# Kernel optimization log

Hardware: AMD Instinct MI355X
Metric: run time of the kernel (lower is better)

The kernel has to match this reference:

```python
import jax, jax.numpy as jnp
import numpy as np
import math

B = 2000000
TWO_PI = 2.0 * math.pi

# ---- e3nn so3 generator construction (numpy, done once at import) ----

def _su2_generators(j):
    m = np.arange(-j, j)
    raising = np.diag(-np.sqrt(j * (j + 1) - m * (m + 1)), k=-1).astype(np.complex128)
    m = np.arange(-j + 1, j + 1)
    lowering = np.diag(np.sqrt(j * (j + 1) - m * (m - 1)), k=1).astype(np.complex128)
    m = np.arange(-j, j + 1)
    return np.stack([0.5 * (raising + lowering), np.diag(1j * m), -0.5j * (raising - lowering)])

def _change_basis_real_to_complex(l):
    q = np.zeros((2 * l + 1, 2 * l + 1), dtype=np.complex128)
    for m in range(-l, 0):
        q[l + m, l + abs(m)] = 1 / 2 ** 0.5
        q[l + m, l - abs(m)] = -1j / 2 ** 0.5
    q[l, l] = 1
    for m in range(1, l + 1):
        q[l + m, l + abs(m)] = (-1) ** m / 2 ** 0.5
        q[l + m, l - abs(m)] = 1j * (-1) ** m / 2 ** 0.5
    return (-1j) ** l * q

def _so3_generators(l):
    X = _su2_generators(l)
    Q = _change_basis_real_to_complex(l)
    return np.real(np.conj(Q.T) @ X @ Q)  # (3, 2l+1, 2l+1); X[0]=x-gen, X[1]=y-gen

def _eig_decomp(X):
    # X real antisymmetric with exact eigenvalues i*m; exp(a*X) = V diag(e^{a w}) V^-1
    w, V = np.linalg.eig(X.astype(np.complex128))
    w = 1j * np.round(w.imag)  # snap to exact i*m
    Vinv = np.linalg.inv(V)
    return (jnp.asarray(w, jnp.complex64), jnp.asarray(V, jnp.complex64), jnp.asarray(Vinv, jnp.complex64))

_GEN = {}
for _l in (4, 6):
    _X = _so3_generators(_l)
    _GEN[_l] = (_eig_decomp(_X[1]), _eig_decomp(_X[0]))  # (y-generator, x-generator)

# ---- rotations / angles (e3nn conventions) ----

def _quat_to_matrix(q):
    # e3nn: angle = 2*acos(clamp(w)), axis = normalize(q[1:]), Rodrigues
    angle = 2.0 * jnp.arccos(jnp.clip(q[..., 0], -1.0, 1.0))
    axis = q[..., 1:]
    axis = axis / jnp.maximum(jnp.linalg.norm(axis, axis=-1, keepdims=True), 1e-12)
    x, y, z = axis[..., 0], axis[..., 1], axis[..., 2]
    c, s = jnp.cos(angle), jnp.sin(angle)
    C = 1.0 - c
    return jnp.stack([
        jnp.stack([c + x * x * C, x * y * C - z * s, x * z * C + y * s], -1),
        jnp.stack([y * x * C + z * s, c + y * y * C, y * z * C - x * s], -1),
        jnp.stack([z * x * C - y * s, z * y * C + x * s, c + z * z * C], -1),
    ], -2)

def _matrix_y(a):
    c, s = jnp.cos(a), jnp.sin(a)
    o, z = jnp.ones_like(a), jnp.zeros_like(a)
    return jnp.stack([jnp.stack([c, z, s], -1), jnp.stack([z, o, z], -1), jnp.stack([-s, z, c], -1)], -2)

def _matrix_x(a):
    c, s = jnp.cos(a), jnp.sin(a)
    o, z = jnp.ones_like(a), jnp.zeros_like(a)
    return jnp.stack([jnp.stack([o, z, z], -1), jnp.stack([z, c, -s], -1), jnp.stack([z, s, c], -1)], -2)

def _xyz_to_angles(xyz):
    n = jnp.linalg.norm(xyz, axis=-1, keepdims=True)
    xyz = jnp.clip(xyz / jnp.maximum(n, 1e-12), -1.0, 1.0)
    beta = jnp.arccos(xyz[..., 1])
    alpha = jnp.arctan2(xyz[..., 0], xyz[..., 2])
    return alpha, beta

def _matrix_to_angles(R):
    x = R[..., :, 1]  # R @ [0,1,0]
    a, b = _xyz_to_angles(x)
    M = jnp.swapaxes(_matrix_y(a) @ _matrix_x(b), -1, -2) @ R
    c = jnp.arctan2(M[..., 0, 2], M[..., 0, 0])
    return a, b, c

# ---- Wigner-D applied to a fixed vector (fused matvec chain) ----

def _rot_apply(decomp, angle, v):
    # exp(angle*X) @ v via precomputed eigendecomposition; result is real
    w, V, Vinv = decomp
    u = jnp.einsum('mj,bj->bm', Vinv, v.astype(jnp.complex64))
    u = u * jnp.exp(angle[:, None].astype(jnp.complex64) * w)
    return jnp.real(jnp.einsum('im,bm->bi', V, u))

def _wigner_apply(l, alpha, beta, gamma, s):
    # D_l(alpha,beta,gamma) @ s = exp(a*Y) exp(b*X) exp(g*Y) @ s
    dy, dx = _GEN[l]
    v = jnp.broadcast_to(s, (alpha.shape[0], s.shape[0]))
    v = _rot_apply(dy, gamma % TWO_PI, v)
    v = _rot_apply(dx, beta % TWO_PI, v)
    v = _rot_apply(dy, alpha % TWO_PI, v)
    return v


def setup_inputs() -> dict:
    key = jax.random.key(0)
    k1, k2, k3 = jax.random.split(key, 3)
    quats = jax.random.normal(k1, (B, 4), dtype=jnp.float32)
    quats = quats / jnp.linalg.norm(quats, axis=-1, keepdims=True)  # unit quaternions
    s4 = jax.random.normal(k2, (9,), dtype=jnp.float32)
    s6 = jax.random.normal(k3, (13,), dtype=jnp.float32)
    return {"quats": quats, "s4": s4, "s6": s6}


def reference(quats, s4, s6):
    R = _quat_to_matrix(quats)
    alpha, beta, gamma = _matrix_to_angles(R)
    f4 = _wigner_apply(4, alpha, beta, gamma, s4)  # (B, 9)
    f6 = _wigner_apply(6, alpha, beta, gamma, s6)  # (B, 13)
    return (f4, f6)
```

## Files before the change

### kernel.cpp

```cpp
#include <hip/hip_runtime.h>
#include <math.h>

#define INV_SQRT2 0.70710678118654752440
#define PI_D 3.14159265358979323846

__global__ void build_J(float* __restrict__ ws) {
  const int l = (blockIdx.x == 0) ? 4 : 6;
  const int n = 2 * l + 1;
  const int off = (blockIdx.x == 0) ? 0 : 96;
  const int tid = threadIdx.x;
  __shared__ double Qr[169], Qi[169], Br[169], Bi[169], A[169], T[169], U[169];

  for (int t = tid; t < 169; t += blockDim.x) { Qr[t] = 0.0; Qi[t] = 0.0; }
  __syncthreads();

  if (tid < n) {
    int m = tid - l;
    if (m < 0) {
      Qr[tid * n + (l - m)] = INV_SQRT2;
      Qi[tid * n + (l + m)] = -INV_SQRT2;
    } else if (m == 0) {
      Qr[tid * n + l] = 1.0;
    } else {
      double sgn = (m & 1) ? -1.0 : 1.0;
      Qr[tid * n + (l + m)] = sgn * INV_SQRT2;
      Qi[tid * n + (l - m)] = sgn * INV_SQRT2;
    }
  }
  __syncthreads();

  if (tid < n * n) {
    int i = tid / n, j = tid % n;
    double br = 0.0, bi = 0.0;
    if (i + 1 < n) {
      double m = (double)(i - l);
      double v = 0.5 * sqrt((double)(l * (l + 1)) - m * (m + 1.0));
      br += v * Qr[(i + 1) * n + j];
      bi += v * Qi[(i + 1) * n + j];
    }
    if (i - 1 >= 0) {
      double m = (double)(i - 1 - l);
      double v = -0.5 * sqrt((double)(l * (l + 1)) - m * (m + 1.0));
      br += v * Qr[(i - 1) * n + j];
      bi += v * Qi[(i - 1) * n + j];
    }
    Br[tid] = br;
    Bi[tid] = bi;
  }
  __syncthreads();

  if (tid < n * n) {
    int i = tid / n, j = tid % n;
    double acc = 0.0;
    for (int k = 0; k < n; k++)
      acc += Qr[k * n + i] * Br[k * n + j] + Qi[k * n + i] * Bi[k * n + j];
    if (j == 2 * l - i && i != l) acc += (double)(l - i);
    A[tid] = acc * (PI_D * INV_SQRT2) * (1.0 / 256.0);
  }
  __syncthreads();

  if (tid < n * n) T[tid] = (tid % (n + 1) == 0) ? 1.0 : 0.0;
  __syncthreads();
  for (int k = 12; k >= 1; k--) {
    if (tid < n * n) {
      int i = tid / n, j = tid % n;
      double acc = 0.0;
      for (int q = 0; q < n; q++) acc += A[i * n + q] * T[q * n + j];
      U[tid] = acc;
    }
    __syncthreads();
    if (tid < n * n) T[tid] = ((tid % (n + 1) == 0) ? 1.0 : 0.0) + U[tid] / (double)k;
    __syncthreads();
  }
  for (int it = 0; it < 8; it++) {
    if (tid < n * n) {
      int i = tid / n, j = tid % n;
      double acc = 0.0;
      for (int q = 0; q < n; q++) acc += T[i * n + q] * T[q * n + j];
      U[tid] = acc;
    }
    __syncthreads();
    if (tid < n * n) T[tid] = U[tid];
    __syncthreads();
  }
  if (tid < n * n) ws[off + tid] = (float)T[tid];
}

template <int L>
__device__ __forceinline__ void rotY(float c1, float s1, const float* v, float* o) {
  o[L] = v[L];
  float ck = c1, sk = s1;
#pragma unroll
  for (int k = 1; k <= L; k++) {
    o[L - k] = ck * v[L - k] + sk * v[L + k];
    o[L + k] = -sk * v[L - k] + ck * v[L + k];
    float cn = ck * c1 - sk * s1;
    sk = sk * c1 + ck * s1;
    ck = cn;
  }
}

template <int L>
__device__ __forceinline__ void matJ(const float* __restrict__ Jg, const float* v, float* o) {
  const int n = 2 * L + 1;
#pragma unroll
  for (int i = 0; i < n; i++) {
    float acc = 0.f;
#pragma unroll
    for (int k = 0; k < n; k++) acc = fmaf(Jg[i * n + k], v[k], acc);
    o[i] = acc;
  }
}

template <int L>
__device__ __forceinline__ void wigner_apply(const float* __restrict__ Jg,
                                             const float* __restrict__ svec,
                                             float ca, float sa, float cb, float sb,
                                             float cg, float sg, float* f) {
  const int n = 2 * L + 1;
  float t[2 * L + 1], u[2 * L + 1], sv[2 * L + 1];
#pragma unroll
  for (int k = 0; k < n; k++) sv[k] = svec[k];
  rotY<L>(cg, sg, sv, t);
  matJ<L>(Jg, t, u);
  rotY<L>(cb, sb, u, t);
  matJ<L>(Jg, t, u);
  rotY<L>(ca, sa, u, f);
}

__global__ __launch_bounds__(256) void wigner_main(
    const float4* __restrict__ quats,
    const float* __restrict__ s4,
    const float* __restrict__ s6,
    const float* __restrict__ ws,
    float* __restrict__ out,
    int B) {
  int i = blockIdx.x * 256 + threadIdx.x;
  if (i >= B) return;
  float4 q = quats[i];

  float w = fminf(fmaxf(q.x, -1.f), 1.f);
  float c = 2.f * w * w - 1.f;
  float s = 2.f * w * sqrtf(fmaxf(1.f - w * w, 0.f));
  float an2 = q.y * q.y + q.z * q.z + q.w * q.w;
  float inv = (an2 > 1e-24f) ? rsqrtf(an2) : 1e12f;
  float ax = q.y * inv, ay = q.z * inv, az = q.w * inv;
  float C = 1.f - c;
  float R00 = c + ax * ax * C, R01 = ax * ay * C - az * s, R02 = ax * az * C + ay * s;
  float R20 = az * ax * C - ay * s, R21 = az * ay * C + ax * s, R22 = c + az * az * C;
  float R11 = c + ay * ay * C;

  float vx = R01, vy = R11, vz = R21;
  float n2 = vx * vx + vy * vy + vz * vz;
  float invn = (n2 > 1e-24f) ? rsqrtf(n2) : 1e12f;
  vx = fminf(fmaxf(vx * invn, -1.f), 1.f);
  vy = fminf(fmaxf(vy * invn, -1.f), 1.f);
  vz = fminf(fmaxf(vz * invn, -1.f), 1.f);
  float cb = vy;
  float sb = sqrtf(fmaxf(1.f - cb * cb, 0.f));
  float h2 = vx * vx + vz * vz;
  float ca, sa;
  if (h2 > 1e-30f) { float rh = rsqrtf(h2); ca = vz * rh; sa = vx * rh; }
  else             { ca = 1.f; sa = 0.f; }
  float M00 = ca * R00 - sa * R20;
  float M02 = ca * R02 - sa * R22;
  float g2 = M00 * M00 + M02 * M02;
  float cg, sg;
  if (g2 > 1e-30f) { float rg = rsqrtf(g2); cg = M00 * rg; sg = M02 * rg; }
  else             { cg = 1.f; sg = 0.f; }

  float f4[9];
  wigner_apply<4>(ws, s4, ca, sa, cb, sb, cg, sg, f4);
  float* o4 = out + (size_t)i * 9;
#pragma unroll
  for (int j = 0; j < 9; j++) o4[j] = f4[j];

  float f6[13];
  wigner_apply<6>(ws + 96, s6, ca, sa, cb, sb, cg, sg, f6);
  float* o6 = out + (size_t)B * 9 + (size_t)i * 13;
#pragma unroll
  for (int j = 0; j < 13; j++) o6[j] = f6[j];
}

extern "C" void kernel_launch(void* const* d_in, const int* in_sizes, int n_in,
                              void* d_out, int out_size, void* d_ws, size_t ws_size,
                              hipStream_t stream) {
  const float4* quats = (const float4*)d_in[0];
  const float* s4 = (const float*)d_in[1];
  const float* s6 = (const float*)d_in[2];
  float* out = (float*)d_out;
  float* ws = (float*)d_ws;
  int B = in_sizes[0] / 4;

  hipLaunchKernelGGL(build_J, dim3(2), dim3(256), 0, stream, ws);
  int blocks = (B + 255) / 256;
  hipLaunchKernelGGL(wigner_main, dim3(blocks), dim3(256), 0, stream,
                     quats, s4, s6, ws, out, B);
}
```

Baseline: 239.9 us.

## Bake J matrices at compile time and stage outputs through LDS for coalesced stores

Replaces the runtime build_J kernel with constexpr construction of the fixed J matrices, so they become compile-time constants. Because the entries are now known to the compiler, zero entries can be skipped in the matrix-vector products. The per-thread strided output writes of 9 and 13 floats are staged through shared memory so each block writes its contiguous output region with coalesced stores. This removes one kernel launch, the constant-matrix loads and the uncoalesced stores. In exchange it costs extra LDS traffic, a barrier and higher LDS usage per block, which may limit occupancy.

Result: faster. 198.4 us (-17.3%).

```diff
diff --git a/kernel.cpp b/kernel.cpp
--- a/kernel.cpp
+++ b/kernel.cpp
@@ -4,87 +4,89 @@
 #define INV_SQRT2 0.70710678118654752440
 #define PI_D 3.14159265358979323846
 
-__global__ void build_J(float* __restrict__ ws) {
-  const int l = (blockIdx.x == 0) ? 4 : 6;
-  const int n = 2 * l + 1;
-  const int off = (blockIdx.x == 0) ? 0 : 96;
-  const int tid = threadIdx.x;
-  __shared__ double Qr[169], Qi[169], Br[169], Bi[169], A[169], T[169], U[169];
-
-  for (int t = tid; t < 169; t += blockDim.x) { Qr[t] = 0.0; Qi[t] = 0.0; }
-  __syncthreads();
-
-  if (tid < n) {
-    int m = tid - l;
+template <int N> struct MatF { float a[N * N]; };
+
+constexpr double csqrt(double x) {
+  if (x <= 0.0) return 0.0;
+  double g = x > 1.0 ? x : 1.0;
+  for (int i = 0; i < 40; ++i) g = 0.5 * (g + x / g);
+  return g;
+}
+
+template <int L>
+constexpr MatF<2 * L + 1> makeJ() {
+  constexpr int n = 2 * L + 1;
+  double Qr[n * n] = {}, Qi[n * n] = {};
+  for (int r = 0; r < n; ++r) {
+    int m = r - L;
     if (m < 0) {
-      Qr[tid * n + (l - m)] = INV_SQRT2;
-      Qi[tid * n + (l + m)] = -INV_SQRT2;
+      Qr[r * n + (L - m)] = INV_SQRT2;
+      Qi[r * n + (L + m)] = -INV_SQRT2;
     } else if (m == 0) {
-      Qr[tid * n + l] = 1.0;
+      Qr[r * n + L] = 1.0;
     } else {
       double sgn = (m & 1) ? -1.0 : 1.0;
-      Qr[tid * n + (l + m)] = sgn * INV_SQRT2;
-      Qi[tid * n + (l - m)] = sgn * INV_SQRT2;
-    }
-  }
-  __syncthreads();
-
-  if (tid < n * n) {
-    int i = tid / n, j = tid % n;
-    double br = 0.0, bi = 0.0;
-    if (i + 1 < n) {
-      double m = (double)(i - l);
-      double v = 0.5 * sqrt((double)(l * (l + 1)) - m * (m + 1.0));
-      br += v * Qr[(i + 1) * n + j];
-      bi += v * Qi[(i + 1) * n + j];
-    }
-    if (i - 1 >= 0) {
-      double m = (double)(i - 1 - l);
-      double v = -0.5 * sqrt((double)(l * (l + 1)) - m * (m + 1.0));
-      br += v * Qr[(i - 1) * n + j];
-      bi += v * Qi[(i - 1) * n + j];
-    }
-    Br[tid] = br;
-    Bi[tid] = bi;
-  }
-  __syncthreads();
-
-  if (tid < n * n) {
-    int i = tid / n, j = tid % n;
-    double acc = 0.0;
-    for (int k = 0; k < n; k++)
-      acc += Qr[k * n + i] * Br[k * n + j] + Qi[k * n + i] * Bi[k * n + j];
-    if (j == 2 * l - i && i != l) acc += (double)(l - i);
-    A[tid] = acc * (PI_D * INV_SQRT2) * (1.0 / 256.0);
-  }
-  __syncthreads();
-
-  if (tid < n * n) T[tid] = (tid % (n + 1) == 0) ? 1.0 : 0.0;
-  __syncthreads();
-  for (int k = 12; k >= 1; k--) {
-    if (tid < n * n) {
-      int i = tid / n, j = tid % n;
-      double acc = 0.0;
-      for (int q = 0; q < n; q++) acc += A[i * n + q] * T[q * n + j];
-      U[tid] = acc;
-    }
-    __syncthreads();
-    if (tid < n * n) T[tid] = ((tid % (n + 1) == 0) ? 1.0 : 0.0) + U[tid] / (double)k;
-    __syncthreads();
-  }
-  for (int it = 0; it < 8; it++) {
-    if (tid < n * n) {
-      int i = tid / n, j = tid % n;
-      double acc = 0.0;
-      for (int q = 0; q < n; q++) acc += T[i * n + q] * T[q * n + j];
-      U[tid] = acc;
-    }
-    __syncthreads();
-    if (tid < n * n) T[tid] = U[tid];
-    __syncthreads();
-  }
-  if (tid < n * n) ws[off + tid] = (float)T[tid];
-}
+      Qr[r * n + (L + m)] = sgn * INV_SQRT2;
+      Qi[r * n + (L - m)] = sgn * INV_SQRT2;
+    }
+  }
+  double c[n] = {};
+  for (int i = 0; i + 1 < n; ++i) {
+    double m = (double)(i - L);
+    c[i] = 0.5 * csqrt((double)(L * (L + 1)) - m * (m + 1.0));
+  }
+  double Br[n * n] = {}, Bi[n * n] = {};
+  for (int i = 0; i < n; ++i)
+    for (int j = 0; j < n; ++j) {
+      double br = 0, bi = 0;
+      if (i + 1 < n) { br += c[i] * Qr[(i + 1) * n + j]; bi += c[i] * Qi[(i + 1) * n + j]; }
+      if (i >= 1)    { br -= c[i - 1] * Qr[(i - 1) * n + j]; bi -= c[i - 1] * Qi[(i - 1) * n + j]; }
+      Br[i * n + j] = br;
+      Bi[i * n + j] = bi;
+    }
+  double A[n * n] = {};
+  for (int i = 0; i < n; ++i)
+    for (int j = 0; j < n; ++j) {
+      double acc = 0;
+      for (int k = 0; k < n; ++k)
+        acc += Qr[k * n + i] * Br[k * n + j] + Qi[k * n + i] * Bi[k * n + j];
+      if (j == 2 * L - i && i != L) acc += (double)(L - i);
+      A[i * n + j] = acc * (PI_D * INV_SQRT2) * (1.0 / 64.0);
+    }
+  double T[n * n] = {}, U[n * n] = {};
+  for (int i = 0; i < n; ++i) T[i * n + i] = 1.0;
+  for (int k = 10; k >= 1; --k) {
+    for (int i = 0; i < n; ++i)
+      for (int j = 0; j < n; ++j) {
+        double acc = 0;
+        for (int q = 0; q < n; ++q) acc += A[i * n + q] * T[q * n + j];
+        U[i * n + j] = acc;
+      }
+    double inv = 1.0 / (double)k;
+    for (int i = 0; i < n; ++i)
+      for (int j = 0; j < n; ++j)
+        T[i * n + j] = ((i == j) ? 1.0 : 0.0) + U[i * n + j] * inv;
+  }
+  for (int s = 0; s < 6; ++s) {
+    for (int i = 0; i < n; ++i)
+      for (int j = 0; j < n; ++j) {
+        double acc = 0;
+        for (int q = 0; q < n; ++q) acc += T[i * n + q] * T[q * n + j];
+        U[i * n + j] = acc;
+      }
+    for (int t = 0; t < n * n; ++t) T[t] = U[t];
+  }
+  MatF<n> R = {};
+  for (int t = 0; t < n * n; ++t) {
+    double v = T[t];
+    if (v < 1e-9 && v > -1e-9) v = 0.0;
+    R.a[t] = (float)v;
+  }
+  return R;
+}
+
+__device__ constexpr MatF<9>  J4 = makeJ<4>();
+__device__ constexpr MatF<13> J6 = makeJ<6>();
 
 template <int L>
 __device__ __forceinline__ void rotY(float c1, float s1, const float* v, float* o) {
@@ -102,12 +104,15 @@
 
 template <int L>
 __device__ __forceinline__ void matJ(const float* __restrict__ Jg, const float* v, float* o) {
-  const int n = 2 * L + 1;
+  constexpr int n = 2 * L + 1;
 #pragma unroll
   for (int i = 0; i < n; i++) {
     float acc = 0.f;
 #pragma unroll
-    for (int k = 0; k < n; k++) acc = fmaf(Jg[i * n + k], v[k], acc);
+    for (int k = 0; k < n; k++) {
+      if (Jg[i * n + k] != 0.0f)
+        acc = fmaf(Jg[i * n + k], v[k], acc);
+    }
     o[i] = acc;
   }
 }
@@ -117,8 +122,8 @@
                                              const float* __restrict__ svec,
                                              float ca, float sa, float cb, float sb,
                                              float cg, float sg, float* f) {
-  const int n = 2 * L + 1;
-  float t[2 * L + 1], u[2 * L + 1], sv[2 * L + 1];
+  constexpr int n = 2 * L + 1;
+  float t[n], u[n], sv[n];
 #pragma unroll
   for (int k = 0; k < n; k++) sv[k] = svec[k];
   rotY<L>(cg, sg, sv, t);
@@ -132,12 +137,14 @@
     const float4* __restrict__ quats,
     const float* __restrict__ s4,
     const float* __restrict__ s6,
-    const float* __restrict__ ws,
     float* __restrict__ out,
     int B) {
-  int i = blockIdx.x * 256 + threadIdx.x;
-  if (i >= B) return;
-  float4 q = quats[i];
+  __shared__ float lds[2304 + 3328];
+  const int t = threadIdx.x;
+  const int b = blockIdx.x;
+  const int i = b * 256 + t;
+  const int idx = (i < B) ? i : (B - 1);
+  float4 q = quats[idx];
 
   float w = fminf(fmaxf(q.x, -1.f), 1.f);
   float c = 2.f * w * w - 1.f;
@@ -170,16 +177,31 @@
   else             { cg = 1.f; sg = 0.f; }
 
   float f4[9];
-  wigner_apply<4>(ws, s4, ca, sa, cb, sb, cg, sg, f4);
-  float* o4 = out + (size_t)i * 9;
-#pragma unroll
-  for (int j = 0; j < 9; j++) o4[j] = f4[j];
-
+  wigner_apply<4>(J4.a, s4, ca, sa, cb, sb, cg, sg, f4);
   float f6[13];
-  wigner_apply<6>(ws + 96, s6, ca, sa, cb, sb, cg, sg, f6);
-  float* o6 = out + (size_t)B * 9 + (size_t)i * 13;
-#pragma unroll
-  for (int j = 0; j < 13; j++) o6[j] = f6[j];
+  wigner_apply<6>(J6.a, s6, ca, sa, cb, sb, cg, sg, f6);
+
+  const bool full = (b + 1) * 256 <= B;
+  if (full) {
+#pragma unroll
+    for (int j = 0; j < 9; j++) lds[t * 9 + j] = f4[j];
+#pragma unroll
+    for (int j = 0; j < 13; j++) lds[2304 + t * 13 + j] = f6[j];
+    __syncthreads();
+    float* o4 = out + (size_t)b * 2304;
+#pragma unroll
+    for (int j = 0; j < 9; j++) o4[j * 256 + t] = lds[j * 256 + t];
+    float* o6 = out + (size_t)B * 9 + (size_t)b * 3328;
+#pragma unroll
+    for (int j = 0; j < 13; j++) o6[j * 256 + t] = lds[2304 + j * 256 + t];
+  } else if (i < B) {
+    float* o4 = out + (size_t)i * 9;
+#pragma unroll
+    for (int j = 0; j < 9; j++) o4[j] = f4[j];
+    float* o6 = out + (size_t)B * 9 + (size_t)i * 13;
+#pragma unroll
+    for (int j = 0; j < 13; j++) o6[j] = f6[j];
+  }
 }
 
 extern "C" void kernel_launch(void* const* d_in, const int* in_sizes, int n_in,
@@ -189,11 +211,8 @@
   const float* s4 = (const float*)d_in[1];
   const float* s6 = (const float*)d_in[2];
   float* out = (float*)d_out;
-  float* ws = (float*)d_ws;
   int B = in_sizes[0] / 4;
-
-  hipLaunchKernelGGL(build_J, dim3(2), dim3(256), 0, stream, ws);
   int blocks = (B + 255) / 256;
   hipLaunchKernelGGL(wigner_main, dim3(blocks), dim3(256), 0, stream,
-                     quats, s4, s6, ws, out, B);
-}
+                     quats, s4, s6, out, B);
+}
```
